# Kernel tuning notes

Hardware: AMD Instinct MI355X
Metric: run time of the kernel (lower is better)

## Reference

```python
import jax, jax.numpy as jnp
import numpy as np

# ---- static configuration (mirrors resource grid / pilot pattern) ----
NB_SYMB = 14                 # num_ofdm_symbols
NSC = 4096                   # fft_size == num_effective_subcarriers (dc_null=False)
PILOT_SYMBS = np.array([2, 11], dtype=np.int32)  # OFDM symbols carrying pilots
STEP = 2                     # subcarriers_step (comb-2, offset 0)
M = NSC // STEP              # pilots per pilot OFDM symbol (constant, as asserted)
BATCH = 512
SC = np.arange(0, NSC, STEP, dtype=np.int32)     # pilot subcarrier positions
ROWS = np.repeat(PILOT_SYMBS, M)                 # flattened pilot (symbol, sc) map,
COLS = np.tile(SC, len(PILOT_SYMBS))             # frequency-then-time ordering


def _time_interp_tables():
    """Replicates _generate_time_interpolation_index_ with numpy (static)."""
    u = PILOT_SYMBS
    idx = np.empty((2, NB_SYMB), dtype=np.int32)
    nf = np.empty(NB_SYMB, dtype=np.float32)
    if u[0] != 0:
        idx[:, : u[0]] = u[0]
        nf[: u[0]] = 0.0
    idx[:, u[-1]:] = u[-1]
    nf[u[-1]:] = 0.0
    for i in range(len(u) - 1):
        idx[0, u[i]: u[i + 1]] = u[i]
        idx[1, u[i]: u[i + 1]] = u[i + 1]
        d = u[i + 1] - u[i]
        nf[u[i]: u[i + 1]] = np.arange(d, dtype=np.float32) / d
    return idx[0], idx[1], nf

IDX0, IDX1, NORM = _time_interp_tables()


def setup_inputs() -> dict:
    key = jax.random.key(0)
    k1, k2 = jax.random.split(key)
    shape = (BATCH, len(PILOT_SYMBS) * M)
    return {
        "h_pilots_real": jax.random.normal(k1, shape, dtype=jnp.float32),
        "h_pilots_imag": jax.random.normal(k2, shape, dtype=jnp.float32),
    }


def reference(h_pilots_real, h_pilots_imag):
    pilots = (h_pilots_real + 1j * h_pilots_imag).astype(jnp.complex64)  # [B, P]
    B = pilots.shape[0]
    # scatter_nd of pilot estimates into the full grid [T, F, B]
    updates = pilots.T  # [P, B]
    grid = jnp.zeros((NB_SYMB, NSC, B), jnp.complex64).at[ROWS, COLS].set(updates)
    # gather pilot OFDM symbols then pilot subcarriers -> [S, M, B]
    est_pilots = grid[PILOT_SYMBS][:, SC, :]
    # M-point unitary DFT along frequency (sionna.signal.fft is ortho-normalized)
    dft = jnp.fft.fft(est_pilots, axis=1, norm="ortho")
    # constant cutoff: fc = floor(M/2)
    fc = M // 2
    padded = jnp.concatenate(
        [
            dft[:, :fc, :],
            jnp.zeros((len(PILOT_SYMBS), NSC - 2 * fc, B), jnp.complex64),
            dft[:, -fc:, :],
        ],
        axis=1,
    )  # [S, NSC, B]
    scaling = jnp.asarray(np.sqrt(np.float32(STEP)), dtype=jnp.complex64)
    freq_interp = scaling * jnp.fft.ifft(padded, axis=1, norm="ortho")
    # scatter interpolated pilot symbols back into the time grid
    interp = jnp.zeros((NB_SYMB, NSC, B), jnp.complex64).at[PILOT_SYMBS].set(freq_interp)
    # time-domain linear interpolation: (H[m+1]-H[m]) * l/L + H[m]
    h0 = interp[IDX0]  # [T, F, B]
    h1 = interp[IDX1]
    norm = jnp.asarray(NORM)[:, None, None]
    out = (h1 - h0) * norm + h0
    # -> [batch, num_ofdm_symbols, num_subcarriers]
    return jnp.transpose(out, (2, 0, 1))
```

## Files before the change

### kernel.cpp

```cpp
#include <hip/hip_runtime.h>
#include <math.h>


#define NSC  4096
#define PI_F 3.14159265358979323846f
#define RSQ2 0.70710678118654752f

__device__ __forceinline__ int pada(int i) { return i + 2 * (i >> 5); }

__device__ __forceinline__ void bf_fwd(float2& a, float2& c, float tc, float ts) {
  const float tx = a.x - c.x, ty = a.y - c.y;
  a.x += c.x; a.y += c.y;
  c.x = tx * tc - ty * ts;
  c.y = tx * ts + ty * tc;
}
__device__ __forceinline__ void bf_inv(float2& a, float2& c, float tc, float ts) {
  const float tx = c.x * tc - c.y * ts, ty = c.x * ts + c.y * tc;
  c.x = a.x - tx; c.y = a.y - ty;
  a.x += tx; a.y += ty;
}

__device__ __forceinline__ void fwd3(float2* x, float c, float s) {
  bf_fwd(x[0], x[4], c, -s);
  { const float cj = RSQ2 * (c - s), sj = RSQ2 * (c + s);
    bf_fwd(x[1], x[5], cj, -sj); }
  bf_fwd(x[2], x[6], -s, -c);
  { const float cj = -RSQ2 * (s + c), sj = RSQ2 * (c - s);
    bf_fwd(x[3], x[7], cj, -sj); }
  const float c2 = c * c - s * s, s2 = 2.f * c * s;
  bf_fwd(x[0], x[2], c2, -s2);  bf_fwd(x[4], x[6], c2, -s2);
  bf_fwd(x[1], x[3], -s2, -c2); bf_fwd(x[5], x[7], -s2, -c2);
  const float c4 = c2 * c2 - s2 * s2, s4 = 2.f * c2 * s2;
  bf_fwd(x[0], x[1], c4, -s4); bf_fwd(x[2], x[3], c4, -s4);
  bf_fwd(x[4], x[5], c4, -s4); bf_fwd(x[6], x[7], c4, -s4);
}

__device__ __forceinline__ void inv3(float2* x, float c, float s) {
  const float c2 = c * c - s * s, s2 = 2.f * c * s;
  const float c4 = c2 * c2 - s2 * s2, s4 = 2.f * c2 * s2;
  bf_inv(x[0], x[1], c4, s4); bf_inv(x[2], x[3], c4, s4);
  bf_inv(x[4], x[5], c4, s4); bf_inv(x[6], x[7], c4, s4);
  bf_inv(x[0], x[2], c2, s2);  bf_inv(x[4], x[6], c2, s2);
  bf_inv(x[1], x[3], -s2, c2); bf_inv(x[5], x[7], -s2, c2);
  bf_inv(x[0], x[4], c, s);
  { const float cj = RSQ2 * (c - s), sj = RSQ2 * (c + s);
    bf_inv(x[1], x[5], cj, sj); }
  bf_inv(x[2], x[6], -s, c);
  { const float cj = -RSQ2 * (s + c), sj = RSQ2 * (c - s);
    bf_inv(x[3], x[7], cj, sj); }
}

__global__ __launch_bounds__(512)
void tdi_fft_interp(const float* __restrict__ in_r,
                    const float* __restrict__ in_i,
                    float4* __restrict__ out) {
  __shared__ __align__(16) float2 A[2][2176];

  const int tid = threadIdx.x;
  const int b   = blockIdx.x;
  const int u   = tid & 255;
  const int sym = tid >> 8;
  float2* __restrict__ As = A[sym];

  const float* __restrict__ pr = in_r + ((size_t)b << 12) + (sym << 11);
  const float* __restrict__ pm = in_i + ((size_t)b << 12) + (sym << 11);

  float2 x[8];
  float s, c;

#pragma unroll
  for (int j = 0; j < 8; ++j)
    x[j] = make_float2(pr[u + 256 * j], pm[u + 256 * j]);
  __sincosf((float)u * (PI_F / 1024.f), &s, &c);
  fwd3(x, c, s);
#pragma unroll
  for (int j = 0; j < 8; ++j) As[pada(u + 256 * j)] = x[j];
  __syncthreads();

  {
    const int q = u & 31;
    const int base = ((u >> 5) << 8) | q;
#pragma unroll
    for (int j = 0; j < 8; ++j) x[j] = As[pada(base + 32 * j)];
    __sincosf((float)q * (PI_F / 128.f), &s, &c);
    fwd3(x, c, s);
#pragma unroll
    for (int j = 0; j < 8; ++j) As[pada(base + 32 * j)] = x[j];
  }
  __syncthreads();

  {
    const int q = u & 3;
    const int base = ((u >> 2) << 5) | q;
#pragma unroll
    for (int j = 0; j < 8; ++j) x[j] = As[pada(base + 4 * j)];
    __sincosf((float)q * (PI_F / 16.f), &s, &c);
    fwd3(x, c, s);
#pragma unroll
    for (int j = 0; j < 8; ++j) As[pada(base + 4 * j)] = x[j];
  }
  __syncthreads();

  {
    const int base = u << 3;
#pragma unroll
    for (int j = 0; j < 8; ++j) x[j] = As[pada(base + j)];
#pragma unroll
    for (int g = 0; g < 8; g += 4) {
      float2 t;
      t.x = x[g].x - x[g+2].x;  t.y = x[g].y - x[g+2].y;
      x[g].x += x[g+2].x;       x[g].y += x[g+2].y;
      x[g+2] = t;
      t.x = x[g+1].x - x[g+3].x; t.y = x[g+1].y - x[g+3].y;
      x[g+1].x += x[g+3].x;      x[g+1].y += x[g+3].y;
      x[g+3] = make_float2(t.y, -t.x);
    }
#pragma unroll
    for (int g = 0; g < 8; g += 2) {
      float2 t;
      t.x = x[g].x - x[g+1].x; t.y = x[g].y - x[g+1].y;
      x[g].x += x[g+1].x;      x[g].y += x[g+1].y;
      x[g+1] = t;
    }
    {
      const float c8[8] = { 1.f,  0.92387953f,  0.70710678f,  0.38268343f,
                            0.f, -0.38268343f, -0.70710678f, -0.92387953f };
      const float s8[8] = { 0.f,  0.38268343f,  0.70710678f,  0.92387953f,
                            1.f,  0.92387953f,  0.70710678f,  0.38268343f };
      float cp, sp;
      __sincosf((float)(__brev((unsigned)u) >> 24) * (PI_F / 2048.f), &sp, &cp);
#pragma unroll
      for (int j = 0; j < 8; ++j) {
        const int rv = ((j & 1) << 2) | (j & 2) | (j >> 2);
        const float sc = (j & 1) ? -(1.f / 2048.f) : (1.f / 2048.f);
        const float fc = (cp * c8[rv] - sp * s8[rv]) * sc;
        const float fs = (sp * c8[rv] + cp * s8[rv]) * sc;
        const float2 a = x[j];
        x[j] = make_float2(a.x * fc - a.y * fs, a.x * fs + a.y * fc);
      }
    }
#pragma unroll
    for (int g = 0; g < 8; g += 2) {
      const float2 t = x[g+1];
      x[g+1].x = x[g].x - t.x; x[g+1].y = x[g].y - t.y;
      x[g].x  += t.x;          x[g].y  += t.y;
    }
#pragma unroll
    for (int g = 0; g < 8; g += 4) {
      float2 t = x[g+2];
      x[g+2].x = x[g].x - t.x; x[g+2].y = x[g].y - t.y;
      x[g].x  += t.x;          x[g].y  += t.y;
      t = make_float2(-x[g+3].y, x[g+3].x);
      x[g+3].x = x[g+1].x - t.x; x[g+3].y = x[g+1].y - t.y;
      x[g+1].x += t.x;           x[g+1].y += t.y;
    }
#pragma unroll
    for (int j = 0; j < 8; ++j) As[pada(base + j)] = x[j];
  }
  __syncthreads();

  {
    const int q = u & 3;
    const int base = ((u >> 2) << 5) | q;
#pragma unroll
    for (int j = 0; j < 8; ++j) x[j] = As[pada(base + 4 * j)];
    __sincosf((float)q * (PI_F / 16.f), &s, &c);
    inv3(x, c, s);
#pragma unroll
    for (int j = 0; j < 8; ++j) As[pada(base + 4 * j)] = x[j];
  }
  __syncthreads();

  {
    const int q = u & 31;
    const int base = ((u >> 5) << 8) | q;
#pragma unroll
    for (int j = 0; j < 8; ++j) x[j] = As[pada(base + 32 * j)];
    __sincosf((float)q * (PI_F / 128.f), &s, &c);
    inv3(x, c, s);
#pragma unroll
    for (int j = 0; j < 8; ++j) As[pada(base + 32 * j)] = x[j];
  }
  __syncthreads();

  {
#pragma unroll
    for (int j = 0; j < 8; ++j) x[j] = As[pada(u + 256 * j)];
    __sincosf((float)u * (PI_F / 1024.f), &s, &c);
    inv3(x, c, s);
#pragma unroll
    for (int j = 0; j < 8; ++j) As[pada(u + 256 * j)] = x[j];
  }
  __syncthreads();

  float2 E0[2], E1[2], O0[2], O1[2];
  const float* __restrict__ er0 = in_r + ((size_t)b << 12);
  const float* __restrict__ er1 = er0 + 2048;
#pragma unroll
  for (int e = 0; e < 2; ++e) {
    const int q = tid + e * 512;
    E0[e] = *(const float2*)&er0[2 * q];
    E1[e] = *(const float2*)&er1[2 * q];
    const float4 a0 = *(const float4*)&A[0][pada(2 * q)];
    const float4 a1 = *(const float4*)&A[1][pada(2 * q)];
    O0[e] = make_float2(a0.x, a0.z);
    O1[e] = make_float2(a1.x, a1.z);
  }
  float4* __restrict__ orow = out + (size_t)b * 14 * 1024;
  for (int t = 0; t < 14; ++t) {
    const float w = (t < 2) ? 0.f : (t >= 11) ? 1.f : (float)(t - 2) * (1.f / 9.f);
#pragma unroll
    for (int e = 0; e < 2; ++e) {
      const int q = tid + e * 512;
      float4 v;
      v.x = E0[e].x + w * (E1[e].x - E0[e].x);
      v.y = O0[e].x + w * (O1[e].x - O0[e].x);
      v.z = E0[e].y + w * (E1[e].y - E0[e].y);
      v.w = O0[e].y + w * (O1[e].y - O0[e].y);
      orow[t * 1024 + q] = v;
    }
  }
}

extern "C" void kernel_launch(void* const* d_in, const int* in_sizes, int n_in,
                              void* d_out, int out_size, void* d_ws, size_t ws_size,
                              hipStream_t stream) {
  const float* hr = (const float*)d_in[0];
  const float* hi = (const float*)d_in[1];
  const int batch = in_sizes[0] / NSC;
  tdi_fft_interp<<<dim3(batch), dim3(512), 0, stream>>>(hr, hi, (float4*)d_out);
}
```

Measured before the change: 131.9 us.

## Split fused FFT-interp kernel into FFT kernel plus separate lerp kernel

Splits the single fused kernel, one 512-thread block per batch row, into two kernels. The first runs one 256-thread block per (batch, pilot symbol) FFT and writes only the real part of the interpolated result to a workspace buffer. The second is a fully parallel elementwise kernel that reads the pilots and the workspace and writes the 14-symbol time interpolation. The aim is better occupancy and more blocks for the store-heavy output phase. The cost is an extra launch and a global round trip through the workspace.

```diff
diff --git a/kernel.cpp b/kernel.cpp
--- a/kernel.cpp
+++ b/kernel.cpp
@@ -50,20 +50,16 @@
     bf_inv(x[3], x[7], cj, sj); }
 }
 
-__global__ __launch_bounds__(512)
-void tdi_fft_interp(const float* __restrict__ in_r,
-                    const float* __restrict__ in_i,
-                    float4* __restrict__ out) {
-  __shared__ __align__(16) float2 A[2][2176];
-
-  const int tid = threadIdx.x;
-  const int b   = blockIdx.x;
-  const int u   = tid & 255;
-  const int sym = tid >> 8;
-  float2* __restrict__ As = A[sym];
-
-  const float* __restrict__ pr = in_r + ((size_t)b << 12) + (sym << 11);
-  const float* __restrict__ pm = in_i + ((size_t)b << 12) + (sym << 11);
+__global__ __launch_bounds__(256)
+void tdi_fft(const float* __restrict__ in_r,
+             const float* __restrict__ in_i,
+             float* __restrict__ ws) {
+  __shared__ __align__(16) float2 As[2176];
+
+  const int u  = threadIdx.x;
+  const int bs = blockIdx.x;
+  const float* __restrict__ pr = in_r + ((size_t)bs << 11);
+  const float* __restrict__ pm = in_i + ((size_t)bs << 11);
 
   float2 x[8];
   float s, c;
@@ -188,37 +184,37 @@
     for (int j = 0; j < 8; ++j) x[j] = As[pada(u + 256 * j)];
     __sincosf((float)u * (PI_F / 1024.f), &s, &c);
     inv3(x, c, s);
-#pragma unroll
-    for (int j = 0; j < 8; ++j) As[pada(u + 256 * j)] = x[j];
-  }
-  __syncthreads();
-
-  float2 E0[2], E1[2], O0[2], O1[2];
-  const float* __restrict__ er0 = in_r + ((size_t)b << 12);
-  const float* __restrict__ er1 = er0 + 2048;
-#pragma unroll
-  for (int e = 0; e < 2; ++e) {
-    const int q = tid + e * 512;
-    E0[e] = *(const float2*)&er0[2 * q];
-    E1[e] = *(const float2*)&er1[2 * q];
-    const float4 a0 = *(const float4*)&A[0][pada(2 * q)];
-    const float4 a1 = *(const float4*)&A[1][pada(2 * q)];
-    O0[e] = make_float2(a0.x, a0.z);
-    O1[e] = make_float2(a1.x, a1.z);
-  }
-  float4* __restrict__ orow = out + (size_t)b * 14 * 1024;
+    float* __restrict__ w = ws + ((size_t)bs << 11);
+#pragma unroll
+    for (int j = 0; j < 8; ++j) w[u + 256 * j] = x[j].x;
+  }
+}
+
+__global__ __launch_bounds__(256)
+void tdi_lerp(const float* __restrict__ in_r,
+              const float* __restrict__ ws,
+              float4* __restrict__ out) {
+  const int g = blockIdx.x * 256 + threadIdx.x;
+  const int b = g >> 10;
+  const int q = g & 1023;
+
+  const float* __restrict__ er = in_r + ((size_t)b << 12);
+  const float* __restrict__ wr = ws   + ((size_t)b << 12);
+  const float2 E0 = *(const float2*)&er[2 * q];
+  const float2 E1 = *(const float2*)&er[2048 + 2 * q];
+  const float2 O0 = *(const float2*)&wr[2 * q];
+  const float2 O1 = *(const float2*)&wr[2048 + 2 * q];
+
+  float4* __restrict__ orow = out + (size_t)b * (14 * 1024) + q;
+#pragma unroll
   for (int t = 0; t < 14; ++t) {
     const float w = (t < 2) ? 0.f : (t >= 11) ? 1.f : (float)(t - 2) * (1.f / 9.f);
-#pragma unroll
-    for (int e = 0; e < 2; ++e) {
-      const int q = tid + e * 512;
-      float4 v;
-      v.x = E0[e].x + w * (E1[e].x - E0[e].x);
-      v.y = O0[e].x + w * (O1[e].x - O0[e].x);
-      v.z = E0[e].y + w * (E1[e].y - E0[e].y);
-      v.w = O0[e].y + w * (O1[e].y - O0[e].y);
-      orow[t * 1024 + q] = v;
-    }
+    float4 v;
+    v.x = E0.x + w * (E1.x - E0.x);
+    v.y = O0.x + w * (O1.x - O0.x);
+    v.z = E0.y + w * (E1.y - E0.y);
+    v.w = O0.y + w * (O1.y - O0.y);
+    orow[(size_t)t * 1024] = v;
   }
 }
 
@@ -228,5 +224,8 @@
   const float* hr = (const float*)d_in[0];
   const float* hi = (const float*)d_in[1];
   const int batch = in_sizes[0] / NSC;
-  tdi_fft_interp<<<dim3(batch), dim3(512), 0, stream>>>(hr, hi, (float4*)d_out);
-}
+  float* ws = (float*)d_ws;
+
+  tdi_fft<<<dim3(batch * 2), dim3(256), 0, stream>>>(hr, hi, ws);
+  tdi_lerp<<<dim3(batch * 4), dim3(256), 0, stream>>>(hr, ws, (float4*)d_out);
+}
```

After: 136.6 us. 3.6% more time.

## Run each 2048-point FFT in one wavefront with register and shuffle stages

Applied to the files above, without the earlier changes.

The block-cooperative shared-memory FFT, with its many barriers, is replaced by one 64-lane wavefront per pilot symbol. Each lane holds 32 points in registers and does the intra-lane radix stages locally, and the cross-lane stages use __shfl_xor, so only one barrier remains before the output stage. The aim is to remove LDS round trips and block-wide synchronisation. In exchange, register pressure rises sharply (64 floats of data per lane plus many sincos twiddles), and each block now has only 128 threads.

```diff
diff --git a/kernel.cpp b/kernel.cpp
--- a/kernel.cpp
+++ b/kernel.cpp
@@ -4,219 +4,139 @@
 
 #define NSC  4096
 #define PI_F 3.14159265358979323846f
-#define RSQ2 0.70710678118654752f
 
-__device__ __forceinline__ int pada(int i) { return i + 2 * (i >> 5); }
-
-__device__ __forceinline__ void bf_fwd(float2& a, float2& c, float tc, float ts) {
-  const float tx = a.x - c.x, ty = a.y - c.y;
-  a.x += c.x; a.y += c.y;
-  c.x = tx * tc - ty * ts;
-  c.y = tx * ts + ty * tc;
-}
-__device__ __forceinline__ void bf_inv(float2& a, float2& c, float tc, float ts) {
-  const float tx = c.x * tc - c.y * ts, ty = c.x * ts + c.y * tc;
-  c.x = a.x - tx; c.y = a.y - ty;
-  a.x += tx; a.y += ty;
+__device__ __forceinline__ float2 cmulf(float2 a, float c, float s) {
+  return make_float2(a.x * c - a.y * s, a.x * s + a.y * c);
 }
 
-__device__ __forceinline__ void fwd3(float2* x, float c, float s) {
-  bf_fwd(x[0], x[4], c, -s);
-  { const float cj = RSQ2 * (c - s), sj = RSQ2 * (c + s);
-    bf_fwd(x[1], x[5], cj, -sj); }
-  bf_fwd(x[2], x[6], -s, -c);
-  { const float cj = -RSQ2 * (s + c), sj = RSQ2 * (c - s);
-    bf_fwd(x[3], x[7], cj, -sj); }
-  const float c2 = c * c - s * s, s2 = 2.f * c * s;
-  bf_fwd(x[0], x[2], c2, -s2);  bf_fwd(x[4], x[6], c2, -s2);
-  bf_fwd(x[1], x[3], -s2, -c2); bf_fwd(x[5], x[7], -s2, -c2);
-  const float c4 = c2 * c2 - s2 * s2, s4 = 2.f * c2 * s2;
-  bf_fwd(x[0], x[1], c4, -s4); bf_fwd(x[2], x[3], c4, -s4);
-  bf_fwd(x[4], x[5], c4, -s4); bf_fwd(x[6], x[7], c4, -s4);
-}
-
-__device__ __forceinline__ void inv3(float2* x, float c, float s) {
-  const float c2 = c * c - s * s, s2 = 2.f * c * s;
-  const float c4 = c2 * c2 - s2 * s2, s4 = 2.f * c2 * s2;
-  bf_inv(x[0], x[1], c4, s4); bf_inv(x[2], x[3], c4, s4);
-  bf_inv(x[4], x[5], c4, s4); bf_inv(x[6], x[7], c4, s4);
-  bf_inv(x[0], x[2], c2, s2);  bf_inv(x[4], x[6], c2, s2);
-  bf_inv(x[1], x[3], -s2, c2); bf_inv(x[5], x[7], -s2, c2);
-  bf_inv(x[0], x[4], c, s);
-  { const float cj = RSQ2 * (c - s), sj = RSQ2 * (c + s);
-    bf_inv(x[1], x[5], cj, sj); }
-  bf_inv(x[2], x[6], -s, c);
-  { const float cj = -RSQ2 * (s + c), sj = RSQ2 * (c - s);
-    bf_inv(x[3], x[7], cj, sj); }
-}
-
-__global__ __launch_bounds__(512)
-void tdi_fft_interp(const float* __restrict__ in_r,
-                    const float* __restrict__ in_i,
-                    float4* __restrict__ out) {
-  __shared__ __align__(16) float2 A[2][2176];
+__global__ __launch_bounds__(128)
+void tdi_wave(const float* __restrict__ in_r,
+              const float* __restrict__ in_i,
+              float4* __restrict__ out) {
+  __shared__ float even_sm[2][2048];
+  __shared__ float odd_sm[2][2048];
 
   const int tid = threadIdx.x;
+  const int l   = tid & 63;
+  const int w   = tid >> 6;
   const int b   = blockIdx.x;
-  const int u   = tid & 255;
-  const int sym = tid >> 8;
-  float2* __restrict__ As = A[sym];
 
-  const float* __restrict__ pr = in_r + ((size_t)b << 12) + (sym << 11);
-  const float* __restrict__ pm = in_i + ((size_t)b << 12) + (sym << 11);
+  const float* __restrict__ pr = in_r + ((size_t)b << 12) + (w << 11);
+  const float* __restrict__ pm = in_i + ((size_t)b << 12) + (w << 11);
 
-  float2 x[8];
-  float s, c;
+  float2 x[32];
 
 #pragma unroll
-  for (int j = 0; j < 8; ++j)
-    x[j] = make_float2(pr[u + 256 * j], pm[u + 256 * j]);
-  __sincosf((float)u * (PI_F / 1024.f), &s, &c);
-  fwd3(x, c, s);
+  for (int r = 0; r < 32; ++r) {
+    const int n = (r << 6) | l;
+    x[r] = make_float2(pr[n], pm[n]);
+    even_sm[w][n] = x[r].x;
+  }
+
 #pragma unroll
-  for (int j = 0; j < 8; ++j) As[pada(u + 256 * j)] = x[j];
+  for (int e = 16; e >= 1; e >>= 1) {
+    const float step = -PI_F / (float)(e * 64);
+#pragma unroll
+    for (int j = 0; j < e; ++j) {
+      float s_, c_;
+      __sincosf(step * (float)(64 * j + l), &s_, &c_);
+#pragma unroll
+      for (int g = 0; g < 32; g += 2 * e) {
+        const int r0 = g + j, r1 = r0 + e;
+        const float2 a = x[r0], bb = x[r1];
+        x[r0] = make_float2(a.x + bb.x, a.y + bb.y);
+        x[r1] = cmulf(make_float2(a.x - bb.x, a.y - bb.y), c_, s_);
+      }
+    }
+  }
+
+#pragma unroll
+  for (int d = 32; d >= 1; d >>= 1) {
+    float s_, c_;
+    __sincosf(-(PI_F / (float)d) * (float)(l & (d - 1)), &s_, &c_);
+    const bool up = (l & d) != 0;
+    const float Wc = up ? c_ : 1.f, Ws = up ? s_ : 0.f;
+    const float sg = up ? -1.f : 1.f;
+#pragma unroll
+    for (int r = 0; r < 32; ++r) {
+      const float px = __shfl_xor(x[r].x, d, 64);
+      const float py = __shfl_xor(x[r].y, d, 64);
+      const float tx = px + sg * x[r].x;
+      const float ty = py + sg * x[r].y;
+      x[r] = make_float2(tx * Wc - ty * Ws, tx * Ws + ty * Wc);
+    }
+  }
+
+  {
+    const int rl6 = (int)(__brev((unsigned)l) >> 26);
+    float sl, cl;
+    __sincosf((PI_F / 64.f) * (float)rl6, &sl, &cl);
+    const float sgn = (l & 1) ? -(1.f / 2048.f) : (1.f / 2048.f);
+#pragma unroll
+    for (int r = 0; r < 32; ++r) {
+      const int rr = (int)(__brev((unsigned)r) >> 27);
+      float sr, cr;
+      __sincosf((PI_F / 2048.f) * (float)rr, &sr, &cr);
+      const float fc = (cl * cr - sl * sr) * sgn;
+      const float fs = (sl * cr + cl * sr) * sgn;
+      x[r] = cmulf(x[r], fc, fs);
+    }
+  }
+
+#pragma unroll
+  for (int d = 1; d <= 32; d <<= 1) {
+    float s_, c_;
+    __sincosf((PI_F / (float)d) * (float)(l & (d - 1)), &s_, &c_);
+    const bool up = (l & d) != 0;
+    const float Wc = up ? c_ : 1.f, Ws = up ? s_ : 0.f;
+    const float sg = up ? -1.f : 1.f;
+#pragma unroll
+    for (int r = 0; r < 32; ++r) {
+      const float yx = x[r].x * Wc - x[r].y * Ws;
+      const float yy = x[r].x * Ws + x[r].y * Wc;
+      const float px = __shfl_xor(yx, d, 64);
+      const float py = __shfl_xor(yy, d, 64);
+      x[r] = make_float2(px + sg * yx, py + sg * yy);
+    }
+  }
+
+#pragma unroll
+  for (int e = 1; e <= 16; e <<= 1) {
+    const float step = PI_F / (float)(e * 64);
+#pragma unroll
+    for (int j = 0; j < e; ++j) {
+      float s_, c_;
+      __sincosf(step * (float)(64 * j + l), &s_, &c_);
+#pragma unroll
+      for (int g = 0; g < 32; g += 2 * e) {
+        const int r0 = g + j, r1 = r0 + e;
+        const float2 t = cmulf(x[r1], c_, s_);
+        x[r1] = make_float2(x[r0].x - t.x, x[r0].y - t.y);
+        x[r0] = make_float2(x[r0].x + t.x, x[r0].y + t.y);
+      }
+    }
+  }
+
+#pragma unroll
+  for (int r = 0; r < 32; ++r) odd_sm[w][(r << 6) | l] = x[r].x;
   __syncthreads();
 
-  {
-    const int q = u & 31;
-    const int base = ((u >> 5) << 8) | q;
+  float4* __restrict__ orow = out + (size_t)b * (14 * 1024);
 #pragma unroll
-    for (int j = 0; j < 8; ++j) x[j] = As[pada(base + 32 * j)];
-    __sincosf((float)q * (PI_F / 128.f), &s, &c);
-    fwd3(x, c, s);
+  for (int e2 = 0; e2 < 8; ++e2) {
+    const int q = tid + (e2 << 7);
+    const float2 E0 = *(const float2*)&even_sm[0][2 * q];
+    const float2 E1 = *(const float2*)&even_sm[1][2 * q];
+    const float2 O0 = *(const float2*)&odd_sm[0][2 * q];
+    const float2 O1 = *(const float2*)&odd_sm[1][2 * q];
 #pragma unroll
-    for (int j = 0; j < 8; ++j) As[pada(base + 32 * j)] = x[j];
-  }
-  __syncthreads();
-
-  {
-    const int q = u & 3;
-    const int base = ((u >> 2) << 5) | q;
-#pragma unroll
-    for (int j = 0; j < 8; ++j) x[j] = As[pada(base + 4 * j)];
-    __sincosf((float)q * (PI_F / 16.f), &s, &c);
-    fwd3(x, c, s);
-#pragma unroll
-    for (int j = 0; j < 8; ++j) As[pada(base + 4 * j)] = x[j];
-  }
-  __syncthreads();
-
-  {
-    const int base = u << 3;
-#pragma unroll
-    for (int j = 0; j < 8; ++j) x[j] = As[pada(base + j)];
-#pragma unroll
-    for (int g = 0; g < 8; g += 4) {
-      float2 t;
-      t.x = x[g].x - x[g+2].x;  t.y = x[g].y - x[g+2].y;
-      x[g].x += x[g+2].x;       x[g].y += x[g+2].y;
-      x[g+2] = t;
-      t.x = x[g+1].x - x[g+3].x; t.y = x[g+1].y - x[g+3].y;
-      x[g+1].x += x[g+3].x;      x[g+1].y += x[g+3].y;
-      x[g+3] = make_float2(t.y, -t.x);
-    }
-#pragma unroll
-    for (int g = 0; g < 8; g += 2) {
-      float2 t;
-      t.x = x[g].x - x[g+1].x; t.y = x[g].y - x[g+1].y;
-      x[g].x += x[g+1].x;      x[g].y += x[g+1].y;
-      x[g+1] = t;
-    }
-    {
-      const float c8[8] = { 1.f,  0.92387953f,  0.70710678f,  0.38268343f,
-                            0.f, -0.38268343f, -0.70710678f, -0.92387953f };
-      const float s8[8] = { 0.f,  0.38268343f,  0.70710678f,  0.92387953f,
-                            1.f,  0.92387953f,  0.70710678f,  0.38268343f };
-      float cp, sp;
-      __sincosf((float)(__brev((unsigned)u) >> 24) * (PI_F / 2048.f), &sp, &cp);
-#pragma unroll
-      for (int j = 0; j < 8; ++j) {
-        const int rv = ((j & 1) << 2) | (j & 2) | (j >> 2);
-        const float sc = (j & 1) ? -(1.f / 2048.f) : (1.f / 2048.f);
-        const float fc = (cp * c8[rv] - sp * s8[rv]) * sc;
-        const float fs = (sp * c8[rv] + cp * s8[rv]) * sc;
-        const float2 a = x[j];
-        x[j] = make_float2(a.x * fc - a.y * fs, a.x * fs + a.y * fc);
-      }
-    }
-#pragma unroll
-    for (int g = 0; g < 8; g += 2) {
-      const float2 t = x[g+1];
-      x[g+1].x = x[g].x - t.x; x[g+1].y = x[g].y - t.y;
-      x[g].x  += t.x;          x[g].y  += t.y;
-    }
-#pragma unroll
-    for (int g = 0; g < 8; g += 4) {
-      float2 t = x[g+2];
-      x[g+2].x = x[g].x - t.x; x[g+2].y = x[g].y - t.y;
-      x[g].x  += t.x;          x[g].y  += t.y;
-      t = make_float2(-x[g+3].y, x[g+3].x);
-      x[g+3].x = x[g+1].x - t.x; x[g+3].y = x[g+1].y - t.y;
-      x[g+1].x += t.x;           x[g+1].y += t.y;
-    }
-#pragma unroll
-    for (int j = 0; j < 8; ++j) As[pada(base + j)] = x[j];
-  }
-  __syncthreads();
-
-  {
-    const int q = u & 3;
-    const int base = ((u >> 2) << 5) | q;
-#pragma unroll
-    for (int j = 0; j < 8; ++j) x[j] = As[pada(base + 4 * j)];
-    __sincosf((float)q * (PI_F / 16.f), &s, &c);
-    inv3(x, c, s);
-#pragma unroll
-    for (int j = 0; j < 8; ++j) As[pada(base + 4 * j)] = x[j];
-  }
-  __syncthreads();
-
-  {
-    const int q = u & 31;
-    const int base = ((u >> 5) << 8) | q;
-#pragma unroll
-    for (int j = 0; j < 8; ++j) x[j] = As[pada(base + 32 * j)];
-    __sincosf((float)q * (PI_F / 128.f), &s, &c);
-    inv3(x, c, s);
-#pragma unroll
-    for (int j = 0; j < 8; ++j) As[pada(base + 32 * j)] = x[j];
-  }
-  __syncthreads();
-
-  {
-#pragma unroll
-    for (int j = 0; j < 8; ++j) x[j] = As[pada(u + 256 * j)];
-    __sincosf((float)u * (PI_F / 1024.f), &s, &c);
-    inv3(x, c, s);
-#pragma unroll
-    for (int j = 0; j < 8; ++j) As[pada(u + 256 * j)] = x[j];
-  }
-  __syncthreads();
-
-  float2 E0[2], E1[2], O0[2], O1[2];
-  const float* __restrict__ er0 = in_r + ((size_t)b << 12);
-  const float* __restrict__ er1 = er0 + 2048;
-#pragma unroll
-  for (int e = 0; e < 2; ++e) {
-    const int q = tid + e * 512;
-    E0[e] = *(const float2*)&er0[2 * q];
-    E1[e] = *(const float2*)&er1[2 * q];
-    const float4 a0 = *(const float4*)&A[0][pada(2 * q)];
-    const float4 a1 = *(const float4*)&A[1][pada(2 * q)];
-    O0[e] = make_float2(a0.x, a0.z);
-    O1[e] = make_float2(a1.x, a1.z);
-  }
-  float4* __restrict__ orow = out + (size_t)b * 14 * 1024;
-  for (int t = 0; t < 14; ++t) {
-    const float w = (t < 2) ? 0.f : (t >= 11) ? 1.f : (float)(t - 2) * (1.f / 9.f);
-#pragma unroll
-    for (int e = 0; e < 2; ++e) {
-      const int q = tid + e * 512;
+    for (int t = 0; t < 14; ++t) {
+      const float wt = (t < 2) ? 0.f : (t >= 11) ? 1.f : (float)(t - 2) * (1.f / 9.f);
       float4 v;
-      v.x = E0[e].x + w * (E1[e].x - E0[e].x);
-      v.y = O0[e].x + w * (O1[e].x - O0[e].x);
-      v.z = E0[e].y + w * (E1[e].y - E0[e].y);
-      v.w = O0[e].y + w * (O1[e].y - O0[e].y);
+      v.x = E0.x + wt * (E1.x - E0.x);
+      v.y = O0.x + wt * (O1.x - O0.x);
+      v.z = E0.y + wt * (E1.y - E0.y);
+      v.w = O0.y + wt * (O1.y - O0.y);
       orow[t * 1024 + q] = v;
     }
   }
@@ -228,5 +148,5 @@
   const float* hr = (const float*)d_in[0];
   const float* hi = (const float*)d_in[1];
   const int batch = in_sizes[0] / NSC;
-  tdi_fft_interp<<<dim3(batch), dim3(512), 0, stream>>>(hr, hi, (float4*)d_out);
+  tdi_wave<<<dim3(batch), dim3(128), 0, stream>>>(hr, hi, (float4*)d_out);
 }
```

New measurement: 146.7 us. +11.2%, slower.

## Pack two real-valued pilot symbols into one complex FFT with Nyquist correction

Applied to the files above, without the earlier changes.

Rather than running two complex 2048-point FFT round trips (one per pilot symbol, 512 threads), the kernel packs the real parts of both pilot symbols into a single complex sequence and runs one FFT/iFFT pass with 256 threads. It exploits the fact that the odd-subcarrier outputs are real-linear and depend only on the real input, and it fixes up the dropped Nyquist bin through an alternating-sign sum reduction (warp shuffles plus a small shared array) that gives alpha/beta offsets. This halves the FFT arithmetic and shared memory per block. In exchange it adds a reduction and relies on a subtle algebraic identity that only holds because the imaginary input affects the output solely through the Nyquist term.

```diff
diff --git a/kernel.cpp b/kernel.cpp
--- a/kernel.cpp
+++ b/kernel.cpp
@@ -50,27 +50,48 @@
     bf_inv(x[3], x[7], cj, sj); }
 }
 
-__global__ __launch_bounds__(512)
-void tdi_fft_interp(const float* __restrict__ in_r,
-                    const float* __restrict__ in_i,
-                    float4* __restrict__ out) {
-  __shared__ __align__(16) float2 A[2][2176];
-
-  const int tid = threadIdx.x;
-  const int b   = blockIdx.x;
-  const int u   = tid & 255;
-  const int sym = tid >> 8;
-  float2* __restrict__ As = A[sym];
-
-  const float* __restrict__ pr = in_r + ((size_t)b << 12) + (sym << 11);
-  const float* __restrict__ pm = in_i + ((size_t)b << 12) + (sym << 11);
+__global__ __launch_bounds__(256)
+void tdi_pk(const float* __restrict__ in_r,
+            const float* __restrict__ in_i,
+            float4* __restrict__ out) {
+  __shared__ __align__(16) float2 As[2176];
+  __shared__ float sred[4][4];
+
+  const int u = threadIdx.x;
+  const int b = blockIdx.x;
+
+  const float* __restrict__ pr0 = in_r + ((size_t)b << 12);
+  const float* __restrict__ pr1 = pr0 + 2048;
+  const float* __restrict__ pi0 = in_i + ((size_t)b << 12);
+  const float* __restrict__ pi1 = pi0 + 2048;
 
   float2 x[8];
   float s, c;
 
-#pragma unroll
-  for (int j = 0; j < 8; ++j)
-    x[j] = make_float2(pr[u + 256 * j], pm[u + 256 * j]);
+  float a_r0 = 0.f, a_r1 = 0.f, a_i0 = 0.f, a_i1 = 0.f;
+#pragma unroll
+  for (int j = 0; j < 8; ++j) {
+    const int n = u + 256 * j;
+    x[j] = make_float2(pr0[n], pr1[n]);
+    a_r0 += x[j].x;  a_r1 += x[j].y;
+    a_i0 += pi0[n];  a_i1 += pi1[n];
+  }
+  {
+    const float sg = (u & 1) ? -1.f : 1.f;
+    a_r0 *= sg; a_r1 *= sg; a_i0 *= sg; a_i1 *= sg;
+#pragma unroll
+    for (int off = 32; off >= 1; off >>= 1) {
+      a_r0 += __shfl_xor(a_r0, off, 64);
+      a_r1 += __shfl_xor(a_r1, off, 64);
+      a_i0 += __shfl_xor(a_i0, off, 64);
+      a_i1 += __shfl_xor(a_i1, off, 64);
+    }
+    if ((u & 63) == 0) {
+      const int w = u >> 6;
+      sred[w][0] = a_r0; sred[w][1] = a_r1;
+      sred[w][2] = a_i0; sred[w][3] = a_i1;
+    }
+  }
   __sincosf((float)u * (PI_F / 1024.f), &s, &c);
   fwd3(x, c, s);
 #pragma unroll
@@ -193,30 +214,30 @@
   }
   __syncthreads();
 
-  float2 E0[2], E1[2], O0[2], O1[2];
-  const float* __restrict__ er0 = in_r + ((size_t)b << 12);
-  const float* __restrict__ er1 = er0 + 2048;
-#pragma unroll
-  for (int e = 0; e < 2; ++e) {
-    const int q = tid + e * 512;
-    E0[e] = *(const float2*)&er0[2 * q];
-    E1[e] = *(const float2*)&er1[2 * q];
-    const float4 a0 = *(const float4*)&A[0][pada(2 * q)];
-    const float4 a1 = *(const float4*)&A[1][pada(2 * q)];
-    O0[e] = make_float2(a0.x, a0.z);
-    O1[e] = make_float2(a1.x, a1.z);
-  }
-  float4* __restrict__ orow = out + (size_t)b * 14 * 1024;
-  for (int t = 0; t < 14; ++t) {
-    const float w = (t < 2) ? 0.f : (t >= 11) ? 1.f : (float)(t - 2) * (1.f / 9.f);
-#pragma unroll
-    for (int e = 0; e < 2; ++e) {
-      const int q = tid + e * 512;
+  const float S0r = sred[0][0] + sred[1][0] + sred[2][0] + sred[3][0];
+  const float S1r = sred[0][1] + sred[1][1] + sred[2][1] + sred[3][1];
+  const float S0i = sred[0][2] + sred[1][2] + sred[2][2] + sred[3][2];
+  const float S1i = sred[0][3] + sred[1][3] + sred[2][3] + sred[3][3];
+  const float alpha = (S0i - S1r) * (1.f / 2048.f);
+  const float beta  = (S0r + S1i) * (1.f / 2048.f);
+
+  float4* __restrict__ orow = out + (size_t)b * (14 * 1024);
+#pragma unroll
+  for (int e = 0; e < 4; ++e) {
+    const int q = u + (e << 8);
+    const float2 E0 = *(const float2*)&pr0[2 * q];
+    const float2 E1 = *(const float2*)&pr1[2 * q];
+    const float4 a  = *(const float4*)&As[pada(2 * q)];
+    const float2 O0 = make_float2(a.x + alpha, a.z - alpha);
+    const float2 O1 = make_float2(a.y + beta,  a.w - beta);
+#pragma unroll
+    for (int t = 0; t < 14; ++t) {
+      const float wt = (t < 2) ? 0.f : (t >= 11) ? 1.f : (float)(t - 2) * (1.f / 9.f);
       float4 v;
-      v.x = E0[e].x + w * (E1[e].x - E0[e].x);
-      v.y = O0[e].x + w * (O1[e].x - O0[e].x);
-      v.z = E0[e].y + w * (E1[e].y - E0[e].y);
-      v.w = O0[e].y + w * (O1[e].y - O0[e].y);
+      v.x = E0.x + wt * (E1.x - E0.x);
+      v.y = O0.x + wt * (O1.x - O0.x);
+      v.z = E0.y + wt * (E1.y - E0.y);
+      v.w = O0.y + wt * (O1.y - O0.y);
       orow[t * 1024 + q] = v;
     }
   }
@@ -228,5 +249,5 @@
   const float* hr = (const float*)d_in[0];
   const float* hi = (const float*)d_in[1];
   const int batch = in_sizes[0] / NSC;
-  tdi_fft_interp<<<dim3(batch), dim3(512), 0, stream>>>(hr, hi, (float4*)d_out);
-}
+  tdi_pk<<<dim3(batch), dim3(256), 0, stream>>>(hr, hi, (float4*)d_out);
+}
```

Result: no change. 134.0 us (+1.6%).
